# Kernel optimization log

Hardware: AMD Instinct MI355X
Metric: run time of the kernel (lower is better)

## Reference

```python
import jax, jax.numpy as jnp
import numpy as np

B, S, UNITS = 32, 2048, 512
D = 2 * UNITS  # 1024


def setup_inputs() -> dict:
    key = jax.random.key(0)
    ks = jax.random.split(key, 12)
    s = 1.0 / np.sqrt(D)
    mask = (jax.random.uniform(ks[0], (B, S)) < 0.9).astype(jnp.float32)
    mask = mask.at[:, 0].set(1.0)  # guarantee no all-zero row
    return {
        "dec_hidden": jax.random.normal(ks[1], (2, B, UNITS), dtype=jnp.float32),
        "enc_output": jax.random.normal(ks[2], (B, S, D), dtype=jnp.float32),
        "enc_pad_mask": mask,
        "prev_coverage": jax.random.uniform(ks[3], (B, S), dtype=jnp.float32) * 0.1,
        "Wh": jax.random.uniform(ks[4], (D, D), minval=-s, maxval=s),
        "bh": jax.random.uniform(ks[5], (D,), minval=-s, maxval=s),
        "Ws": jax.random.uniform(ks[6], (D, D), minval=-s, maxval=s),
        "bs": jax.random.uniform(ks[7], (D,), minval=-s, maxval=s),
        "Wc": jax.random.uniform(ks[8], (D, 1), minval=-1.0, maxval=1.0),
        "bc": jax.random.uniform(ks[9], (D,), minval=-1.0, maxval=1.0),
        "v": jax.random.uniform(ks[10], (1, D), minval=-s, maxval=s),
        "bv": jax.random.uniform(ks[11], (1,), minval=-s, maxval=s),
        "use_coverage": 1,
    }


def reference(dec_hidden, enc_output, enc_pad_mask, prev_coverage,
              Wh, bh, Ws, bs, Wc, bc, v, bv, use_coverage):
    # dec_hidden: (2, B, units) -> (B, 1, 2*units)
    dec = jnp.transpose(dec_hidden, (1, 0, 2)).reshape(dec_hidden.shape[1], 1, -1)
    enc_features = jnp.einsum('bsd,ed->bse', enc_output, Wh) + bh  # (B,S,D)
    dec_features = jnp.einsum('bod,ed->boe', dec, Ws) + bs          # (B,1,D)
    att_inputs = enc_features + dec_features
    if use_coverage:
        # Linear(1 -> D) applied to prev_coverage[..., None]
        coverage_features = prev_coverage[:, :, None] * Wc[:, 0][None, None, :] + bc
        att_inputs = att_inputs + coverage_features
    score = jnp.einsum('bsd,od->bso', jnp.tanh(att_inputs), v) + bv  # (B,S,1)
    attention_weights = jax.nn.softmax(score, axis=1)[..., 0]        # (B,S)
    attention_weights = attention_weights * enc_pad_mask
    attention_weights = attention_weights / jnp.sum(attention_weights, axis=1, keepdims=True)
    context_vector = jnp.einsum('bs,bsd->bd', attention_weights, enc_output)
    if use_coverage:
        coverage_vector = prev_coverage + attention_weights
        return context_vector, attention_weights, coverage_vector
    return context_vector, attention_weights
```

## Files before the change

kernel.cpp:

```cpp
#include <hip/hip_runtime.h>
#include <hip/hip_bf16.h>

#define BATCH 32
#define SEQ   2048
#define DIM   1024

typedef __attribute__((ext_vector_type(4))) float f32x4;
typedef __attribute__((ext_vector_type(8))) short short8;

static __device__ __forceinline__ ushort f2bf(float x) {
    __hip_bfloat16 h = __float2bfloat16(x);
    union { __hip_bfloat16 h; ushort u; } cv; cv.h = h;
    return cv.u;
}

static __device__ __forceinline__ void gll16(const void* g, void* l) {
    __builtin_amdgcn_global_load_lds(
        (const __attribute__((address_space(1))) void*)g,
        (__attribute__((address_space(3))) void*)l, 16, 0, 0);
}

__global__ __launch_bounds__(256) void kAPack(const float* __restrict__ enc,
                                              ushort* __restrict__ apk) {
    int g = blockIdx.x * 256 + threadIdx.x;
    int lane = g & 63;
    int frag = (g >> 6) & 31;
    int kt   = (g >> 11) & 15;
    int strip = g >> 15;
    int mt = frag >> 1, kb = frag & 1;
    int row = (strip << 8) + (mt << 4) + (lane & 15);
    int k0  = (kt << 6) + (kb << 5) + ((lane >> 4) << 3);
    const float* src = enc + (size_t)row * DIM + k0;
    float4 a = *(const float4*)src;
    float4 b = *(const float4*)(src + 4);
    union { ushort us[8]; uint4 u4; } pk;
    pk.us[0] = f2bf(a.x); pk.us[1] = f2bf(a.y); pk.us[2] = f2bf(a.z); pk.us[3] = f2bf(a.w);
    pk.us[4] = f2bf(b.x); pk.us[5] = f2bf(b.y); pk.us[6] = f2bf(b.z); pk.us[7] = f2bf(b.w);
    *(uint4*)(apk + (size_t)g * 8) = pk.u4;
}

__global__ __launch_bounds__(256) void kWhPack(const float* __restrict__ Wh,
                                               ushort* __restrict__ bpk) {
    int g = blockIdx.x * 256 + threadIdx.x;
    int lane = g & 63;
    int frag = (g >> 6) & 31;
    int kt   = (g >> 11) & 15;
    int nb   = g >> 15;
    int ebl = frag >> 1, kbit = frag & 1;
    int e  = (nb << 8) + (ebl << 4) + (lane & 15);
    int k0 = (kt << 6) + (kbit << 5) + ((lane >> 4) << 3);
    const float* src = Wh + (size_t)e * DIM + k0;
    float4 a = *(const float4*)src;
    float4 b = *(const float4*)(src + 4);
    union { ushort us[8]; uint4 u4; } pk;
    pk.us[0] = f2bf(a.x); pk.us[1] = f2bf(a.y); pk.us[2] = f2bf(a.z); pk.us[3] = f2bf(a.w);
    pk.us[4] = f2bf(b.x); pk.us[5] = f2bf(b.y); pk.us[6] = f2bf(b.z); pk.us[7] = f2bf(b.w);
    *(uint4*)(bpk + (size_t)g * 8) = pk.u4;
}

__global__ __launch_bounds__(256) void kBase(const float* __restrict__ dh,
                                             const float* __restrict__ Ws,
                                             const float* __restrict__ bs,
                                             const float* __restrict__ bh,
                                             const float* __restrict__ bc,
                                             const int* __restrict__ uc,
                                             float* __restrict__ base) {
    __shared__ float dec[8][DIM];
    int ec = blockIdx.x >> 2;
    int bg = blockIdx.x & 3;
    int b0 = bg * 8, e0 = ec * 32;
    int tid = threadIdx.x;
    for (int i = tid; i < 8 * DIM; i += 256) {
        int bb = i >> 10, d = i & 1023;
        float vdec = (d < 512) ? dh[(b0 + bb) * 512 + d]
                               : dh[BATCH * 512 + (b0 + bb) * 512 + d - 512];
        dec[bb][d] = vdec;
    }
    __syncthreads();
    int el = tid >> 3, ds = tid & 7;
    int e = e0 + el;
    float acc[8] = {0.f, 0.f, 0.f, 0.f, 0.f, 0.f, 0.f, 0.f};
    const float* wrow = Ws + (size_t)e * DIM;
    for (int i = 0; i < 128; ++i) {
        int d = i * 8 + ds;
        float wv = wrow[d];
#pragma unroll
        for (int bb = 0; bb < 8; ++bb) acc[bb] += wv * dec[bb][d];
    }
#pragma unroll
    for (int bb = 0; bb < 8; ++bb) {
        float s = acc[bb];
        s += __shfl_xor(s, 1); s += __shfl_xor(s, 2); s += __shfl_xor(s, 4);
        acc[bb] = s;
    }
    if (ds == 0) {
        float bias = bs[e] + bh[e] + ((*uc) ? bc[e] : 0.0f);
#pragma unroll
        for (int bb = 0; bb < 8; ++bb) base[(b0 + bb) * DIM + e] = acc[bb] + bias;
    }
}

__global__ __launch_bounds__(512, 2) void kScore(const ushort* __restrict__ apk,
                                                 const ushort* __restrict__ bpk,
                                                 const float* __restrict__ base,
                                                 const float* __restrict__ pc,
                                                 const float* __restrict__ Wc,
                                                 const float* __restrict__ vv,
                                                 const int* __restrict__ uc,
                                                 float* __restrict__ scorep) {
    __shared__ ushort Al[2][16384];
    __shared__ ushort Bl[2][16384];
    __shared__ float red[4][256];

    const int tid = threadIdx.x;
    const int w = tid >> 6, lane = tid & 63;
    const int q = lane >> 4, l15 = lane & 15;
    const int wm = w >> 2, wn = w & 3;

    const int x = blockIdx.x & 7;
    const int j = blockIdx.x >> 3;
    const int ms = (x << 5) + (j >> 2);
    const int nbk = j & 3;
    const int b = ms >> 3;
    const int s0 = (ms & 7) << 8;

    const ushort* abase = apk + ((size_t)ms << 18);
    const ushort* bbase = bpk + ((size_t)nbk << 18);

#define STAGE(KT, BUF) do { \
    const ushort* as_ = abase + ((size_t)(KT) << 14); \
    const ushort* bs_ = bbase + ((size_t)(KT) << 14); \
    _Pragma("unroll") \
    for (int c_ = 0; c_ < 4; ++c_) { \
        int f_ = (c_ << 3) + w; \
        gll16(as_ + (f_ << 9) + (lane << 3), &Al[BUF][f_ << 9]); \
    } \
    _Pragma("unroll") \
    for (int c_ = 0; c_ < 4; ++c_) { \
        int f_ = (c_ << 3) + w; \
        gll16(bs_ + (f_ << 9) + (lane << 3), &Bl[BUF][f_ << 9]); \
    } } while (0)

    f32x4 acc[8][4] = {};

#define KSTEP(BUF) do { \
    _Pragma("unroll") \
    for (int kb = 0; kb < 2; ++kb) { \
        short8 a_[8], b_[4]; \
        _Pragma("unroll") \
        for (int mf = 0; mf < 8; ++mf) \
            a_[mf] = *(const short8*)&Al[BUF][(((((wm << 3) + mf) << 1) + kb) << 9) + (lane << 3)]; \
        _Pragma("unroll") \
        for (int ef = 0; ef < 4; ++ef) \
            b_[ef] = *(const short8*)&Bl[BUF][(((((wn << 2) + ef) << 1) + kb) << 9) + (lane << 3)]; \
        __builtin_amdgcn_s_setprio(1); \
        _Pragma("unroll") \
        for (int ef = 0; ef < 4; ++ef) \
            _Pragma("unroll") \
            for (int mf = 0; mf < 8; ++mf) \
                acc[mf][ef] = __builtin_amdgcn_mfma_f32_16x16x32_bf16(a_[mf], b_[ef], acc[mf][ef], 0, 0, 0); \
        __builtin_amdgcn_s_setprio(0); \
    } } while (0)

    STAGE(0, 0);
    STAGE(1, 1);
    __builtin_amdgcn_sched_barrier(0);
    asm volatile("s_waitcnt vmcnt(8)" ::: "memory");
    __builtin_amdgcn_sched_barrier(0);
    __builtin_amdgcn_s_barrier();
    __builtin_amdgcn_sched_barrier(0);

    for (int t = 0; t < 16; ++t) {
        const int cur = t & 1;
        KSTEP(cur);
        if (t == 15) break;
        __builtin_amdgcn_sched_barrier(0);
        __builtin_amdgcn_s_barrier();
        __builtin_amdgcn_sched_barrier(0);
        if (t < 14) {
            STAGE(t + 2, cur);
            __builtin_amdgcn_sched_barrier(0);
            asm volatile("s_waitcnt vmcnt(8)" ::: "memory");
        } else {
            asm volatile("s_waitcnt vmcnt(0)" ::: "memory");
        }
        __builtin_amdgcn_sched_barrier(0);
        __builtin_amdgcn_s_barrier();
        __builtin_amdgcn_sched_barrier(0);
    }

    const float ucf = (float)(*uc);
    float basee[4], ve[4], wce[4];
#pragma unroll
    for (int ef = 0; ef < 4; ++ef) {
        int e = (nbk << 8) + ((wn << 2) + ef) * 16 + l15;
        basee[ef] = base[b * DIM + e];
        ve[ef] = vv[e];
        wce[ef] = Wc[e] * ucf;
    }
#pragma unroll
    for (int mf = 0; mf < 8; ++mf) {
#pragma unroll
        for (int r = 0; r < 4; ++r) {
            int rl = (wm << 7) + (mf << 4) + (q << 2) + r;
            float p = pc[b * SEQ + s0 + rl];
            float sp = 0.f;
#pragma unroll
            for (int ef = 0; ef < 4; ++ef) {
                float xv = acc[mf][ef][r] + basee[ef] + p * wce[ef];
                float t = 1.0f - 2.0f / (1.0f + __expf(2.0f * xv));
                sp += t * ve[ef];
            }
            sp += __shfl_xor(sp, 1);
            sp += __shfl_xor(sp, 2);
            sp += __shfl_xor(sp, 4);
            sp += __shfl_xor(sp, 8);
            if (l15 == 0) red[wn][rl] = sp;
        }
    }
    __syncthreads();
    if (tid < 256) {
        float s = (red[0][tid] + red[1][tid]) + (red[2][tid] + red[3][tid]);
        scorep[nbk * (BATCH * SEQ) + b * SEQ + s0 + tid] = s;
    }
}

__global__ __launch_bounds__(512) void kSoftmax(const float* __restrict__ scorep,
                                                const float* __restrict__ mask,
                                                const float* __restrict__ pc,
                                                float* __restrict__ att,
                                                float* __restrict__ cov,
                                                int write_cov) {
    __shared__ float rmax[8], rsum[8];
    const int BS = BATCH * SEQ;
    int b = blockIdx.x, tid = threadIdx.x;
    int wv = tid >> 6, ln = tid & 63;
    float x[4];
#pragma unroll
    for (int i = 0; i < 4; ++i) {
        int idx = b * SEQ + tid + i * 512;
        x[i] = (scorep[idx] + scorep[BS + idx]) + (scorep[2 * BS + idx] + scorep[3 * BS + idx]);
    }
    float m = fmaxf(fmaxf(x[0], x[1]), fmaxf(x[2], x[3]));
#pragma unroll
    for (int o = 1; o < 64; o <<= 1) m = fmaxf(m, __shfl_xor(m, o));
    if (ln == 0) rmax[wv] = m;
    __syncthreads();
    m = rmax[0];
#pragma unroll
    for (int i = 1; i < 8; ++i) m = fmaxf(m, rmax[i]);

    float ms[4], wm[4];
#pragma unroll
    for (int i = 0; i < 4; ++i) ms[i] = mask[b * SEQ + tid + i * 512];
    float s = 0.f;
#pragma unroll
    for (int i = 0; i < 4; ++i) { wm[i] = __expf(x[i] - m) * ms[i]; s += wm[i]; }
#pragma unroll
    for (int o = 1; o < 64; o <<= 1) s += __shfl_xor(s, o);
    if (ln == 0) rsum[wv] = s;
    __syncthreads();
    s = 0.f;
#pragma unroll
    for (int i = 0; i < 8; ++i) s += rsum[i];
    float inv = 1.0f / s;
#pragma unroll
    for (int i = 0; i < 4; ++i) {
        float wf = wm[i] * inv;
        att[b * SEQ + tid + i * 512] = wf;
        if (write_cov) cov[b * SEQ + tid + i * 512] = pc[b * SEQ + tid + i * 512] + wf;
    }
}

__global__ __launch_bounds__(256) void kCtxPart(const float* __restrict__ enc,
                                                const float* __restrict__ att,
                                                float* __restrict__ part) {
    __shared__ float wl[64];
    int bx = blockIdx.x;
    int b = bx >> 5, sc = bx & 31;
    int tid = threadIdx.x;
    if (tid < 64) wl[tid] = att[b * SEQ + sc * 64 + tid];
    __syncthreads();
    const float* basep = enc + ((size_t)(b * SEQ + sc * 64)) * DIM + tid * 4;
    float4 acc = {0.f, 0.f, 0.f, 0.f};
#pragma unroll 4
    for (int i = 0; i < 64; ++i) {
        float w = wl[i];
        float4 xv = *(const float4*)(basep + (size_t)i * DIM);
        acc.x += w * xv.x; acc.y += w * xv.y; acc.z += w * xv.z; acc.w += w * xv.w;
    }
    *(float4*)(part + (size_t)bx * DIM + tid * 4) = acc;
}

__global__ __launch_bounds__(256) void kCtxReduce(const float* __restrict__ part,
                                                  float* __restrict__ ctx) {
    int g = blockIdx.x * 256 + threadIdx.x;
    int b = g >> 10, d = g & 1023;
    float s = 0.f;
#pragma unroll
    for (int i = 0; i < 32; ++i) s += part[((size_t)(b * 32 + i) << 10) + d];
    ctx[g] = s;
}

extern "C" void kernel_launch(void* const* d_in, const int* in_sizes, int n_in,
                              void* d_out, int out_size, void* d_ws, size_t ws_size,
                              hipStream_t stream) {
    const float* dh   = (const float*)d_in[0];
    const float* enc  = (const float*)d_in[1];
    const float* mask = (const float*)d_in[2];
    const float* pc   = (const float*)d_in[3];
    const float* Wh   = (const float*)d_in[4];
    const float* bh   = (const float*)d_in[5];
    const float* Ws   = (const float*)d_in[6];
    const float* bs   = (const float*)d_in[7];
    const float* Wc   = (const float*)d_in[8];
    const float* bc   = (const float*)d_in[9];
    const float* vv   = (const float*)d_in[10];
    const int* uc     = (const int*)d_in[12];

    float* ctx = (float*)d_out;
    float* att = ctx + BATCH * DIM;
    float* cov = att + BATCH * SEQ;
    int write_cov = (out_size >= BATCH * (DIM + 2 * SEQ)) ? 1 : 0;

    ushort* apk  = (ushort*)d_ws;
    ushort* bpk  = apk + (size_t)BATCH * SEQ * DIM;
    float* base   = (float*)(bpk + (size_t)DIM * DIM);
    float* scorep = base + BATCH * DIM;
    float* part   = scorep + 4 * BATCH * SEQ;

    kAPack<<<32768, 256, 0, stream>>>(enc, apk);
    kWhPack<<<512, 256, 0, stream>>>(Wh, bpk);
    kBase<<<128, 256, 0, stream>>>(dh, Ws, bs, bh, bc, uc, base);
    kScore<<<1024, 512, 0, stream>>>(apk, bpk, base, pc, Wc, vv, uc, scorep);
    kSoftmax<<<BATCH, 512, 0, stream>>>(scorep, mask, pc, att, cov, write_cov);
    kCtxPart<<<1024, 256, 0, stream>>>(enc, att, part);
    kCtxReduce<<<128, 256, 0, stream>>>(part, ctx);
}
```

Before: 332.5 us.

## Split GEMM main loop into eight interleaved load/MFMA phases per K pair

Replaces the two-stage K loop with a finer schedule of four quadrant phases per K tile. Each phase issues a slice of the next tile's global-to-LDS loads, reads its A/B fragments from LDS into registers, and runs 16 MFMAs between workgroup barriers. The aim is to overlap memory traffic with matrix work at a finer grain and to cut register pressure by holding only half of the A and B fragments at once. In exchange it adds many more s_barrier calls and a full vmcnt(0) drain at the end of each K tile, where the old loop kept loads in flight with vmcnt(8).

```diff
diff --git a/kernel.cpp b/kernel.cpp
--- a/kernel.cpp
+++ b/kernel.cpp
@@ -127,66 +127,78 @@
     const ushort* abase = apk + ((size_t)ms << 18);
     const ushort* bbase = bpk + ((size_t)nbk << 18);
 
-#define STAGE(KT, BUF) do { \
-    const ushort* as_ = abase + ((size_t)(KT) << 14); \
-    const ushort* bs_ = bbase + ((size_t)(KT) << 14); \
-    _Pragma("unroll") \
-    for (int c_ = 0; c_ < 4; ++c_) { \
-        int f_ = (c_ << 3) + w; \
-        gll16(as_ + (f_ << 9) + (lane << 3), &Al[BUF][f_ << 9]); \
-    } \
-    _Pragma("unroll") \
-    for (int c_ = 0; c_ < 4; ++c_) { \
-        int f_ = (c_ << 3) + w; \
-        gll16(bs_ + (f_ << 9) + (lane << 3), &Bl[BUF][f_ << 9]); \
-    } } while (0)
-
+    short8 a_[4][2];
+    short8 b_[2][2];
     f32x4 acc[8][4] = {};
 
-#define KSTEP(BUF) do { \
-    _Pragma("unroll") \
-    for (int kb = 0; kb < 2; ++kb) { \
-        short8 a_[8], b_[4]; \
-        _Pragma("unroll") \
-        for (int mf = 0; mf < 8; ++mf) \
-            a_[mf] = *(const short8*)&Al[BUF][(((((wm << 3) + mf) << 1) + kb) << 9) + (lane << 3)]; \
-        _Pragma("unroll") \
-        for (int ef = 0; ef < 4; ++ef) \
-            b_[ef] = *(const short8*)&Bl[BUF][(((((wn << 2) + ef) << 1) + kb) << 9) + (lane << 3)]; \
-        __builtin_amdgcn_s_setprio(1); \
-        _Pragma("unroll") \
-        for (int ef = 0; ef < 4; ++ef) \
-            _Pragma("unroll") \
-            for (int mf = 0; mf < 8; ++mf) \
-                acc[mf][ef] = __builtin_amdgcn_mfma_f32_16x16x32_bf16(a_[mf], b_[ef], acc[mf][ef], 0, 0, 0); \
-        __builtin_amdgcn_s_setprio(0); \
-    } } while (0)
-
-    STAGE(0, 0);
-    STAGE(1, 1);
-    __builtin_amdgcn_sched_barrier(0);
-    asm volatile("s_waitcnt vmcnt(8)" ::: "memory");
+#define STG_A(KT, BUF, H) do { \
+    const ushort* s_ = abase + ((size_t)(KT) << 14); \
+    int f_ = ((H) << 4) + (w << 1); \
+    gll16(s_ + ((size_t)f_ << 9) + (lane << 3), &Al[BUF][f_ << 9]); \
+    gll16(s_ + ((size_t)(f_ + 1) << 9) + (lane << 3), &Al[BUF][(f_ + 1) << 9]); \
+} while (0)
+
+#define STG_B(KT, BUF, H) do { \
+    const ushort* s_ = bbase + ((size_t)(KT) << 14); \
+    int f_ = ((H) << 4) + (w << 1); \
+    gll16(s_ + ((size_t)f_ << 9) + (lane << 3), &Bl[BUF][f_ << 9]); \
+    gll16(s_ + ((size_t)(f_ + 1) << 9) + (lane << 3), &Bl[BUF][(f_ + 1) << 9]); \
+} while (0)
+
+#define STG_NONE ((void)0)
+
+#define DSA(BUFC, MH, MF, KB) \
+    a_[MF][KB] = *(const short8*)&Al[BUFC][(((((wm << 3) + ((MH) << 2) + (MF)) << 1) + (KB)) << 9) + (lane << 3)]
+#define DSB(BUFC, NH, NB, KB) \
+    b_[NB][KB] = *(const short8*)&Bl[BUFC][(((((wn << 2) + ((NH) << 1) + (NB)) << 1) + (KB)) << 9) + (lane << 3)]
+#define MM(MH, NH, MF, NB, KB) \
+    acc[((MH) << 2) + (MF)][((NH) << 1) + (NB)] = __builtin_amdgcn_mfma_f32_16x16x32_bf16( \
+        a_[MF][KB], b_[NB][KB], acc[((MH) << 2) + (MF)][((NH) << 1) + (NB)], 0, 0, 0)
+
+#define PHASE(BUFC, MH, NH, LA, LB, STG, SEAM) do { \
+    STG; \
+    if (LA) { DSA(BUFC, MH, 0, 0); DSA(BUFC, MH, 0, 1); DSA(BUFC, MH, 1, 0); DSA(BUFC, MH, 1, 1); \
+              DSA(BUFC, MH, 2, 0); DSA(BUFC, MH, 2, 1); DSA(BUFC, MH, 3, 0); DSA(BUFC, MH, 3, 1); } \
+    if (LB) { DSB(BUFC, NH, 0, 0); DSB(BUFC, NH, 0, 1); DSB(BUFC, NH, 1, 0); DSB(BUFC, NH, 1, 1); } \
+    __builtin_amdgcn_sched_barrier(0); \
+    __builtin_amdgcn_s_barrier(); \
+    __builtin_amdgcn_sched_barrier(0); \
+    __builtin_amdgcn_s_setprio(1); \
+    MM(MH, NH, 0, 0, 0); MM(MH, NH, 1, 0, 0); MM(MH, NH, 2, 0, 0); MM(MH, NH, 3, 0, 0); \
+    MM(MH, NH, 0, 1, 0); MM(MH, NH, 1, 1, 0); MM(MH, NH, 2, 1, 0); MM(MH, NH, 3, 1, 0); \
+    MM(MH, NH, 0, 0, 1); MM(MH, NH, 1, 0, 1); MM(MH, NH, 2, 0, 1); MM(MH, NH, 3, 0, 1); \
+    MM(MH, NH, 0, 1, 1); MM(MH, NH, 1, 1, 1); MM(MH, NH, 2, 1, 1); MM(MH, NH, 3, 1, 1); \
+    __builtin_amdgcn_s_setprio(0); \
+    if (SEAM) { asm volatile("s_waitcnt vmcnt(0)" ::: "memory"); } \
+    __builtin_amdgcn_sched_barrier(0); \
+    __builtin_amdgcn_s_barrier(); \
+    __builtin_amdgcn_sched_barrier(0); \
+} while (0)
+
+    STG_A(0, 0, 0); STG_A(0, 0, 1); STG_B(0, 0, 0); STG_B(0, 0, 1);
+    asm volatile("s_waitcnt vmcnt(0)" ::: "memory");
     __builtin_amdgcn_sched_barrier(0);
     __builtin_amdgcn_s_barrier();
     __builtin_amdgcn_sched_barrier(0);
 
-    for (int t = 0; t < 16; ++t) {
-        const int cur = t & 1;
-        KSTEP(cur);
-        if (t == 15) break;
-        __builtin_amdgcn_sched_barrier(0);
-        __builtin_amdgcn_s_barrier();
-        __builtin_amdgcn_sched_barrier(0);
-        if (t < 14) {
-            STAGE(t + 2, cur);
-            __builtin_amdgcn_sched_barrier(0);
-            asm volatile("s_waitcnt vmcnt(8)" ::: "memory");
+    for (int t = 0; t < 8; ++t) {
+        const int to = 2 * t + 1;
+        const int tn = 2 * t + 2;
+        PHASE(0, 0, 0, 1, 1, STG_A(to, 1, 0), 0);
+        PHASE(0, 0, 1, 0, 1, STG_A(to, 1, 1), 0);
+        PHASE(0, 1, 1, 1, 0, STG_B(to, 1, 0), 0);
+        PHASE(0, 1, 0, 0, 1, STG_B(to, 1, 1), 1);
+        if (t < 7) {
+            PHASE(1, 0, 0, 1, 1, STG_A(tn, 0, 0), 0);
+            PHASE(1, 0, 1, 0, 1, STG_A(tn, 0, 1), 0);
+            PHASE(1, 1, 1, 1, 0, STG_B(tn, 0, 0), 0);
+            PHASE(1, 1, 0, 0, 1, STG_B(tn, 0, 1), 1);
         } else {
-            asm volatile("s_waitcnt vmcnt(0)" ::: "memory");
+            PHASE(1, 0, 0, 1, 1, STG_NONE, 0);
+            PHASE(1, 0, 1, 0, 1, STG_NONE, 0);
+            PHASE(1, 1, 1, 1, 0, STG_NONE, 0);
+            PHASE(1, 1, 0, 0, 1, STG_NONE, 0);
         }
-        __builtin_amdgcn_sched_barrier(0);
-        __builtin_amdgcn_s_barrier();
-        __builtin_amdgcn_sched_barrier(0);
     }
 
     const float ucf = (float)(*uc);
@@ -208,8 +220,8 @@
 #pragma unroll
             for (int ef = 0; ef < 4; ++ef) {
                 float xv = acc[mf][ef][r] + basee[ef] + p * wce[ef];
-                float t = 1.0f - 2.0f / (1.0f + __expf(2.0f * xv));
-                sp += t * ve[ef];
+                float tt = 1.0f - 2.0f / (1.0f + __expf(2.0f * xv));
+                sp += tt * ve[ef];
             }
             sp += __shfl_xor(sp, 1);
             sp += __shfl_xor(sp, 2);
```

Result: slower. 669.0 us (+101.2%).
